# Kernel tuning notes

Hardware: AMD Instinct MI355X
Metric: run time of the kernel (lower is better)

Reference implementation:

```python
import jax, jax.numpy as jnp
import numpy as np

WINDOW = 7
NUM_HEADS = 16
HEAD_DIM = 32  # dim=512 / 16 heads
SCALE = HEAD_DIM ** -0.5


def _relative_position_index(ws: int) -> np.ndarray:
    ch, cw = np.meshgrid(np.arange(ws), np.arange(ws), indexing='ij')
    coords = np.stack([ch, cw]).reshape(2, -1)            # [2, ws*ws]
    rel = coords[:, :, None] - coords[:, None, :]          # [2, N, N]
    rel = rel.transpose(1, 2, 0)                           # [N, N, 2]
    rel[:, :, 0] += ws - 1
    rel[:, :, 1] += ws - 1
    rel[:, :, 0] *= 2 * ws - 1
    return rel.sum(-1)                                     # [N, N]

REL_IDX = jnp.asarray(_relative_position_index(WINDOW))   # [49, 49] int


def setup_inputs() -> dict:
    key = jax.random.key(0)
    ks = jax.random.split(key, 6)
    B, N, C = 2048, WINDOW * WINDOW, NUM_HEADS * HEAD_DIM
    return {
        'hidden_states': jax.random.normal(ks[0], (B, N, C), jnp.float32),
        'attention_mask': jnp.zeros((B, N, N), jnp.float32),
        'qkv_w': jax.random.normal(ks[1], (3 * C, C), jnp.float32) * 0.02,
        'qkv_b': jax.random.normal(ks[2], (3 * C,), jnp.float32) * 0.02,
        'out_w': jax.random.normal(ks[3], (C, C), jnp.float32) * 0.02,
        'out_b': jax.random.normal(ks[4], (C,), jnp.float32) * 0.02,
        'rel_pos_table': jax.random.normal(ks[5], ((2 * WINDOW - 1) ** 2, NUM_HEADS), jnp.float32) * 0.02,
    }


def reference(hidden_states, attention_mask, qkv_w, qkv_b, out_w, out_b, rel_pos_table):
    B, N, C = hidden_states.shape
    H, D = NUM_HEADS, HEAD_DIM
    qkv = hidden_states @ qkv_w.T + qkv_b                  # [B, N, 3C]
    q, k, v = jnp.split(qkv, 3, axis=-1)
    q = q.reshape(B, N, H, D).transpose(0, 2, 1, 3)        # [B, H, N, D]
    k = k.reshape(B, N, H, D).transpose(0, 2, 1, 3)
    v = v.reshape(B, N, H, D).transpose(0, 2, 1, 3)
    attn = jnp.einsum('bhnd,bhmd->bhnm', q, k) * SCALE     # [B, H, N, N]
    # relative position bias: gather [N*N] rows -> [N, N, H] -> [1, H, N, N]
    bias = rel_pos_table[REL_IDX.reshape(-1)].reshape(N, N, H).transpose(2, 0, 1)
    attn = attn + bias[None] + attention_mask[:, None]
    attn = jax.nn.softmax(attn, axis=-1)                   # dropout = identity (eval)
    out = jnp.einsum('bhnm,bhmd->bhnd', attn, v)           # [B, H, N, D]
    out = out.transpose(0, 2, 1, 3).reshape(B, N, C)
    return out @ out_w.T + out_b
```

## Files before the change

### kernel.cpp

```cpp
#include <hip/hip_runtime.h>
#include <hip/hip_bf16.h>

typedef __attribute__((ext_vector_type(8))) __bf16 bf16x8;
typedef __attribute__((ext_vector_type(4))) __bf16 bf16x4;
typedef __attribute__((ext_vector_type(4))) float f32x4;

#define MFMA16(a,b,c) __builtin_amdgcn_mfma_f32_16x16x32_bf16(a,b,c,0,0,0)

__device__ __forceinline__ void gload_lds16(const void* g, void* l) {
  __builtin_amdgcn_global_load_lds(
      (const __attribute__((address_space(1))) void*)g,
      (__attribute__((address_space(3))) void*)l, 16, 0, 0);
}

__device__ __forceinline__ f32x4 max4(f32x4 a, f32x4 b) {
  f32x4 c;
  c[0] = fmaxf(a[0], b[0]); c[1] = fmaxf(a[1], b[1]);
  c[2] = fmaxf(a[2], b[2]); c[3] = fmaxf(a[3], b[3]);
  return c;
}

__global__ void prep_k(const float* __restrict__ qkv_w, const float* __restrict__ out_w,
                       const float* __restrict__ rpt,
                       __bf16* __restrict__ qwb, __bf16* __restrict__ owb,
                       __bf16* __restrict__ biasb)
{
  int i = blockIdx.x * 256 + threadIdx.x;
  if (i < 786432) { qwb[i] = (__bf16)qkv_w[i]; return; }
  i -= 786432;
  if (i < 262144) { owb[i] = (__bf16)out_w[i]; return; }
  i -= 262144;
  if (i < 65536) {
    int hh = i >> 12, qc = i & 4095, qq = qc >> 6, c = qc & 63;
    __bf16 val;
    if (c >= 49)      val = (__bf16)(-30000.0f);
    else if (qq >= 49) val = (__bf16)(0.0f);
    else {
      int dh = qq / 7 - c / 7 + 6;
      int dw = qq % 7 - c % 7 + 6;
      val = (__bf16)rpt[(dh * 13 + dw) * 16 + hh];
    }
    biasb[i] = val;
  }
}

__global__ void cast_k(const float* __restrict__ in, __bf16* __restrict__ outb, int n8)
{
  int i = blockIdx.x * blockDim.x + threadIdx.x;
  int stride = gridDim.x * blockDim.x;
  for (; i < n8; i += stride) {
    const float4* p = (const float4*)in + (size_t)i * 2;
    float4 x = p[0], y = p[1];
    bf16x8 o;
    o[0] = (__bf16)x.x; o[1] = (__bf16)x.y; o[2] = (__bf16)x.z; o[3] = (__bf16)x.w;
    o[4] = (__bf16)y.x; o[5] = (__bf16)y.y; o[6] = (__bf16)y.z; o[7] = (__bf16)y.w;
    ((bf16x8*)outb)[i] = o;
  }
}

template<int EPI>
__global__ __launch_bounds__(256, 3)
void gemm_bt(const __bf16* __restrict__ A, const __bf16* __restrict__ Bt,
             const float* __restrict__ bvec, float* __restrict__ outp,
             __bf16* __restrict__ qb, __bf16* __restrict__ kb, __bf16* __restrict__ vb,
             int M, int N, int K)
{
  __shared__ __bf16 As[128 * 32];
  __shared__ __bf16 Bs[128 * 32];
  const int tid  = threadIdx.x;
  const int wave = tid >> 6, lane = tid & 63;
  const int g = lane >> 4, r = lane & 15;
  const int ntiles = N >> 7;
  const int m0 = (blockIdx.x / ntiles) << 7;
  const int n0 = (blockIdx.x % ntiles) << 7;
  const int wr = wave >> 1, wc = wave & 1;

  f32x4 acc[4][4] = {};

  const char* gA = (const char*)A + ((size_t)(m0 + (wave << 4) + (lane >> 2)) * K + (lane & 3) * 8) * 2;
  const char* gB = (const char*)Bt + ((size_t)(n0 + (wave << 4) + (lane >> 2)) * K + (lane & 3) * 8) * 2;
  char* lA = (char*)As + wave * 1024;
  char* lB = (char*)Bs + wave * 1024;
  const size_t rowskip = (size_t)64 * K * 2;

  for (int k0 = 0; k0 < K; k0 += 32) {
    __syncthreads();
    gload_lds16(gA, lA);
    gload_lds16(gA + rowskip, lA + 4096);
    gload_lds16(gB, lB);
    gload_lds16(gB + rowskip, lB + 4096);
    gA += 64; gB += 64;
    __syncthreads();

    bf16x8 af[4], bfr[4];
#pragma unroll
    for (int mi = 0; mi < 4; ++mi)
      af[mi] = *(const bf16x8*)((const char*)As + ((wr * 64 + mi * 16 + r) * 32 + g * 8) * 2);
#pragma unroll
    for (int ni = 0; ni < 4; ++ni)
      bfr[ni] = *(const bf16x8*)((const char*)Bs + ((wc * 64 + ni * 16 + r) * 32 + g * 8) * 2);
#pragma unroll
    for (int mi = 0; mi < 4; ++mi)
#pragma unroll
      for (int ni = 0; ni < 4; ++ni)
        acc[mi][ni] = MFMA16(af[mi], bfr[ni], acc[mi][ni]);
  }

  if (EPI == 1) {
#pragma unroll
    for (int mi = 0; mi < 4; ++mi) {
      int row = m0 + wr * 64 + mi * 16 + g * 4;
#pragma unroll
      for (int ni = 0; ni < 4; ++ni) {
        int col = n0 + wc * 64 + ni * 16 + r;
        float bv = bvec[col];
#pragma unroll
        for (int j = 0; j < 4; ++j)
          outp[(size_t)(row + j) * N + col] = acc[mi][ni][j] + bv;
      }
    }
  } else {
    __bf16* dst; float scl;
    const int which = n0 >> 9;
    if (which == 0)      { dst = qb; scl = 0.17677669529663687f; }
    else if (which == 1) { dst = kb; scl = 1.0f; }
    else                 { dst = vb; scl = 1.0f; }
#pragma unroll
    for (int mi = 0; mi < 4; ++mi) {
#pragma unroll
      for (int ni = 0; ni < 4; ++ni) {
        int n = n0 + wc * 64 + ni * 16 + r;
        float bv = bvec[n];
        int nl = n & 511;
        int hh = nl >> 5, d = nl & 31;
#pragma unroll
        for (int j = 0; j < 4; ++j) {
          int m = m0 + wr * 64 + mi * 16 + g * 4 + j;
          int bb = m / 49, t = m - bb * 49;
          float val = (acc[mi][ni][j] + bv) * scl;
          dst[(((size_t)bb * 16 + hh) * 49 + t) * 32 + d] = (__bf16)val;
        }
      }
    }
  }
}

__global__ __launch_bounds__(256, 4)
void attn_k(const __bf16* __restrict__ qb, const __bf16* __restrict__ kb,
            const __bf16* __restrict__ vb, const __bf16* __restrict__ bias_p,
            const float* __restrict__ mask, __bf16* __restrict__ ao)
{
  __shared__ float maskl[64 * 64];
  __shared__ __bf16 Vt[4][32 * 64];
  __shared__ __bf16 Pl[4][16 * 64];
  const int tid = threadIdx.x, wave = tid >> 6, lane = tid & 63;
  const int g = lane >> 4, r = lane & 15;
  const int b = blockIdx.x >> 2, hg = blockIdx.x & 3;
  const int h = hg * 4 + wave;
  const size_t bh = (size_t)b * 16 + h;
  const __bf16* q = qb + bh * 1568;
  const __bf16* k = kb + bh * 1568;
  const __bf16* v = vb + bh * 1568;
  const bf16x8 z8 = {};
  const f32x4 z4 = {};

  bf16x8* vtz = (bf16x8*)Vt[wave];
#pragma unroll
  for (int i = 0; i < 4; ++i) vtz[i * 64 + lane] = z8;

  const float* mb = mask + (size_t)b * 2401;
#pragma unroll
  for (int i = 0; i < 16; ++i) {
    int idx = i * 256 + tid;
    int qq = idx >> 6, c = idx & 63;
    float mv = (qq < 49 && c < 49) ? mb[qq * 49 + c] : 0.0f;
    maskl[qq * 64 + (c ^ ((qq & 7) << 2))] = mv;
  }

  bf16x8 kf[4], qf[4];
#pragma unroll
  for (int i = 0; i < 4; ++i) {
    int row = i * 16 + r;
    kf[i] = (row < 49) ? *(const bf16x8*)(k + row * 32 + g * 8) : z8;
    qf[i] = (row < 49) ? *(const bf16x8*)(q + row * 32 + g * 8) : z8;
  }

  __syncthreads();

  char* vt = (char*)Vt[wave];
#pragma unroll
  for (int i = 0; i < 4; ++i) {
    int idx = i * 64 + lane;
    int t = idx >> 2, d0 = (idx & 3) << 3;
    if (t < 49) {
      bf16x8 vv = *(const bf16x8*)(v + t * 32 + d0);
#pragma unroll
      for (int j = 0; j < 8; ++j) {
        int d = d0 + j;
        *(__bf16*)(vt + d * 128 + ((t * 2) ^ ((d & 7) << 4))) = vv[j];
      }
    }
  }

  bf16x8 vf[2][2];
#pragma unroll
  for (int di = 0; di < 2; ++di) {
    int row = di * 16 + r;
#pragma unroll
    for (int t = 0; t < 2; ++t)
      vf[di][t] = *(const bf16x8*)(vt + row * 128 + (((t * 32 + g * 8) * 2) ^ ((row & 7) << 4)));
  }

  const __bf16* bp = bias_p + h * 4096;
  char* pw = (char*)Pl[wave];
  __bf16* aob = ao + (size_t)b * 25088 + h * 32;
  const int swz = (r & 7) << 4;
  const int mswz = (r & 7) << 2;

#pragma unroll
  for (int qi = 0; qi < 4; ++qi) {
    f32x4 s[4];
#pragma unroll
    for (int mi = 0; mi < 4; ++mi) s[mi] = MFMA16(kf[mi], qf[qi], z4);

    const int qrow = qi * 16 + r;
#pragma unroll
    for (int mi = 0; mi < 4; ++mi) {
      int c0 = mi * 16 + g * 4;
      bf16x4 b4 = *(const bf16x4*)(bp + qrow * 64 + c0);
      f32x4 m4 = *(const f32x4*)(maskl + qrow * 64 + (c0 ^ mswz));
#pragma unroll
      for (int jj = 0; jj < 4; ++jj)
        s[mi][jj] += (float)b4[jj] + m4[jj];
    }
    f32x4 a = max4(max4(s[0], s[1]), max4(s[2], s[3]));
    float mx = fmaxf(fmaxf(a[0], a[1]), fmaxf(a[2], a[3]));
    mx = fmaxf(mx, __shfl_xor(mx, 16));
    mx = fmaxf(mx, __shfl_xor(mx, 32));
    float sum = 0.0f;
#pragma unroll
    for (int mi = 0; mi < 4; ++mi) {
#pragma unroll
      for (int jj = 0; jj < 4; ++jj) {
        float e = __expf(s[mi][jj] - mx);
        s[mi][jj] = e;
        sum += e;
      }
    }
    sum += __shfl_xor(sum, 16);
    sum += __shfl_xor(sum, 32);
    const float rinv = 1.0f / sum;

#pragma unroll
    for (int mi = 0; mi < 4; ++mi) {
      bf16x4 w;
#pragma unroll
      for (int jj = 0; jj < 4; ++jj) w[jj] = (__bf16)(s[mi][jj] * rinv);
      *(bf16x4*)(pw + r * 128 + (((mi * 16 + g * 4) * 2) ^ swz)) = w;
    }
    bf16x8 pa0 = *(const bf16x8*)(pw + r * 128 + ((g * 16) ^ swz));
    bf16x8 pa1 = *(const bf16x8*)(pw + r * 128 + ((64 + g * 16) ^ swz));

#pragma unroll
    for (int di = 0; di < 2; ++di) {
      f32x4 o = MFMA16(pa0, vf[di][0], z4);
      o = MFMA16(pa1, vf[di][1], o);
#pragma unroll
      for (int jj = 0; jj < 4; ++jj) {
        int qq = qi * 16 + g * 4 + jj;
        if (qq < 49)
          aob[(size_t)qq * 512 + di * 16 + r] = (__bf16)o[jj];
      }
    }
  }
}

extern "C" void kernel_launch(void* const* d_in, const int* in_sizes, int n_in,
                              void* d_out, int out_size, void* d_ws, size_t ws_size,
                              hipStream_t stream)
{
  const float* hs    = (const float*)d_in[0];
  const float* mask  = (const float*)d_in[1];
  const float* qkv_w = (const float*)d_in[2];
  const float* qkv_b = (const float*)d_in[3];
  const float* out_w = (const float*)d_in[4];
  const float* out_b = (const float*)d_in[5];
  const float* rpt   = (const float*)d_in[6];
  float* out = (float*)d_out;

  char* ws = (char*)d_ws;
  __bf16* hsb  = (__bf16*)(ws);
  __bf16* qb   = (__bf16*)(ws + 102760448);
  __bf16* kb   = (__bf16*)(ws + 205520896);
  __bf16* vb   = (__bf16*)(ws + 308281344);
  __bf16* qwb  = (__bf16*)(ws + 411041792);
  __bf16* owb  = (__bf16*)(ws + 412614656);
  __bf16* biasb= (__bf16*)(ws + 413138944);

  prep_k<<<4352, 256, 0, stream>>>(qkv_w, out_w, rpt, qwb, owb, biasb);
  cast_k<<<2048, 256, 0, stream>>>(hs, hsb, 6422528);
  gemm_bt<0><<<9408, 256, 0, stream>>>(hsb, qwb, qkv_b, nullptr, qb, kb, vb,
                                       100352, 1536, 512);
  attn_k<<<8192, 256, 0, stream>>>(qb, kb, vb, biasb, mask, hsb);
  gemm_bt<1><<<3136, 256, 0, stream>>>(hsb, owb, out_b, out, nullptr, nullptr, nullptr,
                                       100352, 512, 512);
}
```

Baseline: 551.5 us.

## Replace GEMMs with 256x256-tile 8-wave double-buffered pipelined kernel

Both projection GEMMs move from a 128x128 tile with 4 waves and a fully synchronized single LDS buffer to a 256x256 tile with 8 waves. The new kernel double-buffers in 128KB of LDS with XOR-swizzled layout, prefetches two k-steps ahead, and interleaves LDS reads with MFMA using barriers and s_setprio. Blocks are remapped across 8 groups to improve cache locality, and the QKV scatter epilogue hoists the bias loads. The kernel hardcodes K=512 (8 k-steps), and its large LDS footprint limits occupancy to one block per CU.

```diff
diff --git a/kernel.cpp b/kernel.cpp
--- a/kernel.cpp
+++ b/kernel.cpp
@@ -59,57 +59,149 @@
 }
 
 template<int EPI>
-__global__ __launch_bounds__(256, 3)
-void gemm_bt(const __bf16* __restrict__ A, const __bf16* __restrict__ Bt,
-             const float* __restrict__ bvec, float* __restrict__ outp,
-             __bf16* __restrict__ qb, __bf16* __restrict__ kb, __bf16* __restrict__ vb,
-             int M, int N, int K)
+__global__ __launch_bounds__(512, 2)
+void gemm8p(const __bf16* __restrict__ A, const __bf16* __restrict__ Bt,
+            const float* __restrict__ bvec, float* __restrict__ outp,
+            __bf16* __restrict__ qb, __bf16* __restrict__ kb, __bf16* __restrict__ vb,
+            int N, int K)
 {
-  __shared__ __bf16 As[128 * 32];
-  __shared__ __bf16 Bs[128 * 32];
-  const int tid  = threadIdx.x;
+  __shared__ __align__(16) char lds[131072];
+  const int tid = threadIdx.x;
   const int wave = tid >> 6, lane = tid & 63;
   const int g = lane >> 4, r = lane & 15;
-  const int ntiles = N >> 7;
-  const int m0 = (blockIdx.x / ntiles) << 7;
-  const int n0 = (blockIdx.x % ntiles) << 7;
-  const int wr = wave >> 1, wc = wave & 1;
-
-  f32x4 acc[4][4] = {};
-
-  const char* gA = (const char*)A + ((size_t)(m0 + (wave << 4) + (lane >> 2)) * K + (lane & 3) * 8) * 2;
-  const char* gB = (const char*)Bt + ((size_t)(n0 + (wave << 4) + (lane >> 2)) * K + (lane & 3) * 8) * 2;
-  char* lA = (char*)As + wave * 1024;
-  char* lB = (char*)Bs + wave * 1024;
-  const size_t rowskip = (size_t)64 * K * 2;
-
-  for (int k0 = 0; k0 < K; k0 += 32) {
-    __syncthreads();
-    gload_lds16(gA, lA);
-    gload_lds16(gA + rowskip, lA + 4096);
-    gload_lds16(gB, lB);
-    gload_lds16(gB + rowskip, lB + 4096);
-    gA += 64; gB += 64;
-    __syncthreads();
-
-    bf16x8 af[4], bfr[4];
+  const int l8 = lane >> 3, l7 = lane & 7;
+  const int wr = wave >> 2, wc = wave & 3;
+
+  const int ntiles = N >> 8;
+  const int nper = gridDim.x >> 3;
+  const int b2 = (blockIdx.x & 7) * nper + (blockIdx.x >> 3);
+  const int m0 = (b2 / ntiles) << 8;
+  const int n0 = (b2 % ntiles) << 8;
+
+  const __bf16* Ag = A + (size_t)(m0 + wave * 8 + l8) * K + (l7 ^ l8) * 8;
+  const __bf16* Bg = Bt + (size_t)(n0 + wave * 8 + l8) * K + (l7 ^ l8) * 8;
+  const size_t c64 = (size_t)64 * K;
+
+  const int swz = r & 7;
+  const int ch0 = (g ^ swz) << 4;
+  const int ch1 = ((4 + g) ^ swz) << 4;
+  const char* Ar = lds + (wr * 128 + r) * 128;
+  const char* Br = lds + 32768 + (wc * 64 + r) * 128;
+
+  f32x4 acc[8][4] = {};
+  bf16x8 a[4][2], b[4][2];
+
+#pragma unroll
+  for (int c = 0; c < 4; ++c) {
+    gload_lds16(Ag + c * c64, lds + wave * 1024 + c * 8192);
+    gload_lds16(Bg + c * c64, lds + 32768 + wave * 1024 + c * 8192);
+  }
+#pragma unroll
+  for (int c = 0; c < 4; ++c) {
+    gload_lds16(Ag + 64 + c * c64, lds + 65536 + wave * 1024 + c * 8192);
+    gload_lds16(Bg + 64 + c * c64, lds + 65536 + 32768 + wave * 1024 + c * 8192);
+  }
+
+#pragma unroll 1
+  for (int kt = 0; kt < 8; ++kt) {
+    const int cur = (kt & 1) << 16;
+    const char* Ab = Ar + cur;
+    const char* Bb = Br + cur;
+    if (kt == 7) asm volatile("s_waitcnt vmcnt(0)" ::: "memory");
+    else         asm volatile("s_waitcnt vmcnt(8)" ::: "memory");
+    __builtin_amdgcn_s_barrier();
+
+#pragma unroll
+    for (int mi = 0; mi < 4; ++mi) {
+      a[mi][0] = *(const bf16x8*)(Ab + mi * 2048 + ch0);
+      a[mi][1] = *(const bf16x8*)(Ab + mi * 2048 + ch1);
+    }
+#pragma unroll
+    for (int ni = 0; ni < 2; ++ni) {
+      b[ni][0] = *(const bf16x8*)(Bb + ni * 2048 + ch0);
+      b[ni][1] = *(const bf16x8*)(Bb + ni * 2048 + ch1);
+    }
+    __builtin_amdgcn_s_barrier();
+    asm volatile("s_waitcnt lgkmcnt(0)" ::: "memory");
+    __builtin_amdgcn_sched_barrier(0);
+    __builtin_amdgcn_s_setprio(1);
 #pragma unroll
     for (int mi = 0; mi < 4; ++mi)
-      af[mi] = *(const bf16x8*)((const char*)As + ((wr * 64 + mi * 16 + r) * 32 + g * 8) * 2);
-#pragma unroll
-    for (int ni = 0; ni < 4; ++ni)
-      bfr[ni] = *(const bf16x8*)((const char*)Bs + ((wc * 64 + ni * 16 + r) * 32 + g * 8) * 2);
+#pragma unroll
+      for (int ni = 0; ni < 2; ++ni) {
+        acc[mi][ni] = MFMA16(a[mi][0], b[ni][0], acc[mi][ni]);
+        acc[mi][ni] = MFMA16(a[mi][1], b[ni][1], acc[mi][ni]);
+      }
+    __builtin_amdgcn_s_setprio(0);
+    __builtin_amdgcn_s_barrier();
+
+#pragma unroll
+    for (int ni = 2; ni < 4; ++ni) {
+      b[ni][0] = *(const bf16x8*)(Bb + ni * 2048 + ch0);
+      b[ni][1] = *(const bf16x8*)(Bb + ni * 2048 + ch1);
+    }
+    __builtin_amdgcn_s_barrier();
+    asm volatile("s_waitcnt lgkmcnt(0)" ::: "memory");
+    __builtin_amdgcn_sched_barrier(0);
+    __builtin_amdgcn_s_setprio(1);
 #pragma unroll
     for (int mi = 0; mi < 4; ++mi)
 #pragma unroll
-      for (int ni = 0; ni < 4; ++ni)
-        acc[mi][ni] = MFMA16(af[mi], bfr[ni], acc[mi][ni]);
+      for (int ni = 2; ni < 4; ++ni) {
+        acc[mi][ni] = MFMA16(a[mi][0], b[ni][0], acc[mi][ni]);
+        acc[mi][ni] = MFMA16(a[mi][1], b[ni][1], acc[mi][ni]);
+      }
+    __builtin_amdgcn_s_setprio(0);
+    __builtin_amdgcn_s_barrier();
+
+#pragma unroll
+    for (int mi = 0; mi < 4; ++mi) {
+      a[mi][0] = *(const bf16x8*)(Ab + (4 + mi) * 2048 + ch0);
+      a[mi][1] = *(const bf16x8*)(Ab + (4 + mi) * 2048 + ch1);
+    }
+    __builtin_amdgcn_s_barrier();
+    asm volatile("s_waitcnt lgkmcnt(0)" ::: "memory");
+    __builtin_amdgcn_sched_barrier(0);
+    __builtin_amdgcn_s_setprio(1);
+#pragma unroll
+    for (int mi = 0; mi < 4; ++mi)
+#pragma unroll
+      for (int ni = 2; ni < 4; ++ni) {
+        acc[4 + mi][ni] = MFMA16(a[mi][0], b[ni][0], acc[4 + mi][ni]);
+        acc[4 + mi][ni] = MFMA16(a[mi][1], b[ni][1], acc[4 + mi][ni]);
+      }
+    __builtin_amdgcn_s_setprio(0);
+    __builtin_amdgcn_s_barrier();
+
+    if (kt < 6) {
+      const __bf16* Agk = Ag + (kt + 2) * 64;
+      const __bf16* Bgk = Bt == A ? Agk : Bg + (kt + 2) * 64;
+      (void)Bgk;
+      char* Al = lds + cur + wave * 1024;
+      char* Bl = lds + cur + 32768 + wave * 1024;
+      const __bf16* Bgk2 = Bg + (kt + 2) * 64;
+#pragma unroll
+      for (int c = 0; c < 4; ++c) {
+        gload_lds16(Agk + c * c64, Al + c * 8192);
+        gload_lds16(Bgk2 + c * c64, Bl + c * 8192);
+      }
+    }
+    __builtin_amdgcn_s_setprio(1);
+#pragma unroll
+    for (int mi = 0; mi < 4; ++mi)
+#pragma unroll
+      for (int ni = 0; ni < 2; ++ni) {
+        acc[4 + mi][ni] = MFMA16(a[mi][0], b[ni][0], acc[4 + mi][ni]);
+        acc[4 + mi][ni] = MFMA16(a[mi][1], b[ni][1], acc[4 + mi][ni]);
+      }
+    __builtin_amdgcn_s_setprio(0);
+    __builtin_amdgcn_s_barrier();
   }
 
   if (EPI == 1) {
 #pragma unroll
-    for (int mi = 0; mi < 4; ++mi) {
-      int row = m0 + wr * 64 + mi * 16 + g * 4;
+    for (int mi = 0; mi < 8; ++mi) {
+      int row = m0 + wr * 128 + mi * 16 + g * 4;
 #pragma unroll
       for (int ni = 0; ni < 4; ++ni) {
         int col = n0 + wc * 64 + ni * 16 + r;
@@ -125,20 +217,22 @@
     if (which == 0)      { dst = qb; scl = 0.17677669529663687f; }
     else if (which == 1) { dst = kb; scl = 1.0f; }
     else                 { dst = vb; scl = 1.0f; }
-#pragma unroll
-    for (int mi = 0; mi < 4; ++mi) {
-#pragma unroll
-      for (int ni = 0; ni < 4; ++ni) {
-        int n = n0 + wc * 64 + ni * 16 + r;
-        float bv = bvec[n];
-        int nl = n & 511;
-        int hh = nl >> 5, d = nl & 31;
-#pragma unroll
-        for (int j = 0; j < 4; ++j) {
-          int m = m0 + wr * 64 + mi * 16 + g * 4 + j;
-          int bb = m / 49, t = m - bb * 49;
-          float val = (acc[mi][ni][j] + bv) * scl;
-          dst[(((size_t)bb * 16 + hh) * 49 + t) * 32 + d] = (__bf16)val;
+    float bv[4];
+#pragma unroll
+    for (int ni = 0; ni < 4; ++ni) bv[ni] = bvec[n0 + wc * 64 + ni * 16 + r];
+#pragma unroll
+    for (int mi = 0; mi < 8; ++mi) {
+#pragma unroll
+      for (int j = 0; j < 4; ++j) {
+        int m = m0 + wr * 128 + mi * 16 + g * 4 + j;
+        int bb = m / 49, t = m - bb * 49;
+        __bf16* drow = dst + ((size_t)bb * 16) * 1568 + t * 32;
+#pragma unroll
+        for (int ni = 0; ni < 4; ++ni) {
+          int nl = (n0 + wc * 64 + ni * 16 + r) & 511;
+          int hh = nl >> 5, d = nl & 31;
+          float val = (acc[mi][ni][j] + bv[ni]) * scl;
+          drow[(size_t)hh * 1568 + d] = (__bf16)val;
         }
       }
     }
@@ -233,8 +327,8 @@
       for (int jj = 0; jj < 4; ++jj)
         s[mi][jj] += (float)b4[jj] + m4[jj];
     }
-    f32x4 a = max4(max4(s[0], s[1]), max4(s[2], s[3]));
-    float mx = fmaxf(fmaxf(a[0], a[1]), fmaxf(a[2], a[3]));
+    f32x4 aa = max4(max4(s[0], s[1]), max4(s[2], s[3]));
+    float mx = fmaxf(fmaxf(aa[0], aa[1]), fmaxf(aa[2], aa[3]));
     mx = fmaxf(mx, __shfl_xor(mx, 16));
     mx = fmaxf(mx, __shfl_xor(mx, 32));
     float sum = 0.0f;
@@ -299,9 +393,9 @@
 
   prep_k<<<4352, 256, 0, stream>>>(qkv_w, out_w, rpt, qwb, owb, biasb);
   cast_k<<<2048, 256, 0, stream>>>(hs, hsb, 6422528);
-  gemm_bt<0><<<9408, 256, 0, stream>>>(hsb, qwb, qkv_b, nullptr, qb, kb, vb,
-                                       100352, 1536, 512);
+  gemm8p<0><<<2352, 512, 0, stream>>>(hsb, qwb, qkv_b, nullptr, qb, kb, vb,
+                                      1536, 512);
   attn_k<<<8192, 256, 0, stream>>>(qb, kb, vb, biasb, mask, hsb);
-  gemm_bt<1><<<3136, 256, 0, stream>>>(hsb, owb, out_b, out, nullptr, nullptr, nullptr,
-                                       100352, 512, 512);
-}
+  gemm8p<1><<<784, 512, 0, stream>>>(hsb, owb, out_b, out, nullptr, nullptr, nullptr,
+                                     512, 512);
+}
```

New measurement: 526.8 us. -4.5%, faster.

## Restructure GEMMs as persistent blocks holding a full weight strip in LDS

Applied to the files above, without the earlier changes.

Replaces the tiled GEMM with a persistent-style kernel. Each 512-thread block loads one 128-column strip of the weight matrix (full K=512) into 128KB of swizzled LDS once, then loops over many 256-row M tiles. A operands are read straight from global memory into registers with double buffering, and epilogue stores are vectorized. This removes the repeated B reloads and per-k-step barriers. In exchange, occupancy drops to one block per CU, A loads bypass LDS, and the grid is small enough that load balance could suffer.

```diff
diff --git a/kernel.cpp b/kernel.cpp
--- a/kernel.cpp
+++ b/kernel.cpp
@@ -59,90 +59,120 @@
 }
 
 template<int EPI>
-__global__ __launch_bounds__(256, 3)
-void gemm_bt(const __bf16* __restrict__ A, const __bf16* __restrict__ Bt,
-             const float* __restrict__ bvec, float* __restrict__ outp,
-             __bf16* __restrict__ qb, __bf16* __restrict__ kb, __bf16* __restrict__ vb,
-             int M, int N, int K)
-{
-  __shared__ __bf16 As[128 * 32];
-  __shared__ __bf16 Bs[128 * 32];
-  const int tid  = threadIdx.x;
+__global__ __launch_bounds__(512, 1)
+void gemmbs(const __bf16* __restrict__ A, const __bf16* __restrict__ Bt,
+            const float* __restrict__ bvec, float* __restrict__ outp,
+            __bf16* __restrict__ qb, __bf16* __restrict__ kb, __bf16* __restrict__ vb,
+            int nstrips, int groups)
+{
+  __shared__ __align__(16) char ldsB[131072];
+  const int tid = threadIdx.x;
   const int wave = tid >> 6, lane = tid & 63;
   const int g = lane >> 4, r = lane & 15;
-  const int ntiles = N >> 7;
-  const int m0 = (blockIdx.x / ntiles) << 7;
-  const int n0 = (blockIdx.x % ntiles) << 7;
   const int wr = wave >> 1, wc = wave & 1;
-
-  f32x4 acc[4][4] = {};
-
-  const char* gA = (const char*)A + ((size_t)(m0 + (wave << 4) + (lane >> 2)) * K + (lane & 3) * 8) * 2;
-  const char* gB = (const char*)Bt + ((size_t)(n0 + (wave << 4) + (lane >> 2)) * K + (lane & 3) * 8) * 2;
-  char* lA = (char*)As + wave * 1024;
-  char* lB = (char*)Bs + wave * 1024;
-  const size_t rowskip = (size_t)64 * K * 2;
-
-  for (int k0 = 0; k0 < K; k0 += 32) {
+  const int strip = blockIdx.x % nstrips;
+  const int mg = blockIdx.x / nstrips;
+
+  {
+    const __bf16* Bg = Bt + (size_t)strip * 128 * 512;
+#pragma unroll
+    for (int i = 0; i < 16; ++i) {
+      int n = i * 8 + wave;
+      gload_lds16(Bg + (size_t)n * 512 + (lane ^ wave) * 8,
+                  ldsB + i * 8192 + tid * 16);
+    }
+    asm volatile("s_waitcnt vmcnt(0)" ::: "memory");
     __syncthreads();
-    gload_lds16(gA, lA);
-    gload_lds16(gA + rowskip, lA + 4096);
-    gload_lds16(gB, lB);
-    gload_lds16(gB + rowskip, lB + 4096);
-    gA += 64; gB += 64;
-    __syncthreads();
-
-    bf16x8 af[4], bfr[4];
-#pragma unroll
-    for (int mi = 0; mi < 4; ++mi)
-      af[mi] = *(const bf16x8*)((const char*)As + ((wr * 64 + mi * 16 + r) * 32 + g * 8) * 2);
-#pragma unroll
-    for (int ni = 0; ni < 4; ++ni)
-      bfr[ni] = *(const bf16x8*)((const char*)Bs + ((wc * 64 + ni * 16 + r) * 32 + g * 8) * 2);
-#pragma unroll
-    for (int mi = 0; mi < 4; ++mi)
-#pragma unroll
-      for (int ni = 0; ni < 4; ++ni)
-        acc[mi][ni] = MFMA16(af[mi], bfr[ni], acc[mi][ni]);
-  }
-
-  if (EPI == 1) {
-#pragma unroll
-    for (int mi = 0; mi < 4; ++mi) {
-      int row = m0 + wr * 64 + mi * 16 + g * 4;
-#pragma unroll
-      for (int ni = 0; ni < 4; ++ni) {
-        int col = n0 + wc * 64 + ni * 16 + r;
-        float bv = bvec[col];
-#pragma unroll
-        for (int j = 0; j < 4; ++j)
-          outp[(size_t)(row + j) * N + col] = acc[mi][ni][j] + bv;
-      }
-    }
-  } else {
-    __bf16* dst; float scl;
-    const int which = n0 >> 9;
-    if (which == 0)      { dst = qb; scl = 0.17677669529663687f; }
-    else if (which == 1) { dst = kb; scl = 1.0f; }
-    else                 { dst = vb; scl = 1.0f; }
-#pragma unroll
-    for (int mi = 0; mi < 4; ++mi) {
-#pragma unroll
-      for (int ni = 0; ni < 4; ++ni) {
-        int n = n0 + wc * 64 + ni * 16 + r;
-        float bv = bvec[n];
-        int nl = n & 511;
-        int hh = nl >> 5, d = nl & 31;
-#pragma unroll
-        for (int j = 0; j < 4; ++j) {
-          int m = m0 + wr * 64 + mi * 16 + g * 4 + j;
-          int bb = m / 49, t = m - bb * 49;
-          float val = (acc[mi][ni][j] + bv) * scl;
-          dst[(((size_t)bb * 16 + hh) * 49 + t) * 32 + d] = (__bf16)val;
+  }
+
+  int bbase[4], bswz[4];
+#pragma unroll
+  for (int ni = 0; ni < 4; ++ni) {
+    int nloc = wc * 64 + ni * 16 + r;
+    bbase[ni] = nloc * 1024;
+    bswz[ni] = nloc & 7;
+  }
+
+  f32x4 bv4[4];
+#pragma unroll
+  for (int ni = 0; ni < 4; ++ni)
+    bv4[ni] = *(const f32x4*)(bvec + strip * 128 + wc * 64 + ni * 16 + g * 4);
+
+  __bf16* dst = qb; float scl = 0.17677669529663687f;
+  int hh_[4], d0_[4];
+  if (EPI == 0) {
+    const int which = strip >> 2;
+    if (which == 1)      { dst = kb; scl = 1.0f; }
+    else if (which == 2) { dst = vb; scl = 1.0f; }
+#pragma unroll
+    for (int ni = 0; ni < 4; ++ni) {
+      int nl = (strip * 128 + wc * 64 + ni * 16) & 511;
+      hh_[ni] = nl >> 5;
+      d0_[ni] = (nl & 31) + g * 4;
+    }
+  }
+
+#define LOADA(S, KT) { _Pragma("unroll")                                       \
+  for (int mi_ = 0; mi_ < 4; ++mi_) {                                          \
+    S[mi_][0] = *(const bf16x8*)(ap + mi_ * 8192 + (KT) * 64);                 \
+    S[mi_][1] = *(const bf16x8*)(ap + mi_ * 8192 + (KT) * 64 + 32); } }
+
+#define DOKT(S, KT) { bf16x8 bf_[4][2];                                        \
+  _Pragma("unroll")                                                            \
+  for (int ni_ = 0; ni_ < 4; ++ni_) {                                          \
+    bf_[ni_][0] = *(const bf16x8*)(ldsB + bbase[ni_] +                         \
+                    ((((KT) * 8 + g) ^ bswz[ni_]) << 4));                      \
+    bf_[ni_][1] = *(const bf16x8*)(ldsB + bbase[ni_] +                         \
+                    ((((KT) * 8 + 4 + g) ^ bswz[ni_]) << 4)); }                \
+  _Pragma("unroll")                                                            \
+  for (int mi_ = 0; mi_ < 4; ++mi_)                                            \
+    _Pragma("unroll")                                                          \
+    for (int ni_ = 0; ni_ < 4; ++ni_) {                                        \
+      acc[mi_][ni_] = MFMA16(bf_[ni_][0], S[mi_][0], acc[mi_][ni_]);           \
+      acc[mi_][ni_] = MFMA16(bf_[ni_][1], S[mi_][1], acc[mi_][ni_]); } }
+
+  for (int mt = mg; mt < 392; mt += groups) {
+    const __bf16* ap = A + ((size_t)mt * 256 + wr * 64 + r) * 512 + g * 8;
+    f32x4 acc[4][4] = {};
+    bf16x8 aX[4][2], aY[4][2];
+
+    LOADA(aX, 0)
+#pragma unroll
+    for (int kt = 0; kt < 8; ++kt) {
+      if (kt < 7) { if (kt & 1) LOADA(aX, kt + 1) else LOADA(aY, kt + 1) }
+      if (kt & 1) DOKT(aY, kt) else DOKT(aX, kt)
+    }
+
+    if (EPI == 1) {
+#pragma unroll
+      for (int mi = 0; mi < 4; ++mi) {
+        int m = mt * 256 + wr * 64 + mi * 16 + r;
+        float* orow = outp + (size_t)m * 512 + strip * 128 + wc * 64 + g * 4;
+#pragma unroll
+        for (int ni = 0; ni < 4; ++ni) {
+          f32x4 w = acc[mi][ni] + bv4[ni];
+          *(f32x4*)(orow + ni * 16) = w;
         }
       }
-    }
-  }
+    } else {
+#pragma unroll
+      for (int mi = 0; mi < 4; ++mi) {
+        int m = mt * 256 + wr * 64 + mi * 16 + r;
+        int bb = m / 49, t49 = m - bb * 49;
+        __bf16* dr = dst + (size_t)bb * 25088 + t49 * 32;
+#pragma unroll
+        for (int ni = 0; ni < 4; ++ni) {
+          f32x4 v = acc[mi][ni];
+          bf16x4 w;
+#pragma unroll
+          for (int j = 0; j < 4; ++j) w[j] = (__bf16)((v[j] + bv4[ni][j]) * scl);
+          *(bf16x4*)(dr + hh_[ni] * 1568 + d0_[ni]) = w;
+        }
+      }
+    }
+  }
+#undef LOADA
+#undef DOKT
 }
 
 __global__ __launch_bounds__(256, 4)
@@ -233,8 +263,8 @@
       for (int jj = 0; jj < 4; ++jj)
         s[mi][jj] += (float)b4[jj] + m4[jj];
     }
-    f32x4 a = max4(max4(s[0], s[1]), max4(s[2], s[3]));
-    float mx = fmaxf(fmaxf(a[0], a[1]), fmaxf(a[2], a[3]));
+    f32x4 aa = max4(max4(s[0], s[1]), max4(s[2], s[3]));
+    float mx = fmaxf(fmaxf(aa[0], aa[1]), fmaxf(aa[2], aa[3]));
     mx = fmaxf(mx, __shfl_xor(mx, 16));
     mx = fmaxf(mx, __shfl_xor(mx, 32));
     float sum = 0.0f;
@@ -299,9 +329,7 @@
 
   prep_k<<<4352, 256, 0, stream>>>(qkv_w, out_w, rpt, qwb, owb, biasb);
   cast_k<<<2048, 256, 0, stream>>>(hs, hsb, 6422528);
-  gemm_bt<0><<<9408, 256, 0, stream>>>(hsb, qwb, qkv_b, nullptr, qb, kb, vb,
-                                       100352, 1536, 512);
+  gemmbs<0><<<768, 512, 0, stream>>>(hsb, qwb, qkv_b, nullptr, qb, kb, vb, 12, 64);
   attn_k<<<8192, 256, 0, stream>>>(qb, kb, vb, biasb, mask, hsb);
-  gemm_bt<1><<<3136, 256, 0, stream>>>(hsb, owb, out_b, out, nullptr, nullptr, nullptr,
-                                       100352, 512, 512);
-}
+  gemmbs<1><<<256, 512, 0, stream>>>(hsb, owb, out_b, out, nullptr, nullptr, nullptr, 4, 64);
+}
```

Result: slower. 1.141 ms (+106.8%).
